# Kernel optimization log

Measured on AMD Instinct MI355X. Metric: run time of the kernel, lower is better.

## Reference

```python
import jax, jax.numpy as jnp
import numpy as np

L = 256
UP = 2
# ktype -> (rotations, ((pad_top,pad_bot),(pad_left,pad_right)), (b_row_off, b_col_off))
CONFIG = {
    'h': ([0, 2],        ((0, 0), (0, 1)), (0, 1)),
    'd': ([0, 1, 2, 3],  ((0, 1), (0, 1)), (1, 1)),
    'v': ([0, 2],        ((0, 1), (0, 0)), (1, 0)),
}


def setup_inputs() -> dict:
    key = jax.random.key(0)
    k0, k1, k2, k3 = jax.random.split(key, 4)
    img_lr = jax.random.randint(k0, (32, 1, 512, 512), 0, L, dtype=jnp.int32)
    h_weight = jax.random.normal(k1, (L * L, UP * UP), dtype=jnp.float32)
    d_weight = jax.random.normal(k2, (L * L, UP * UP), dtype=jnp.float32)
    v_weight = jax.random.normal(k3, (L * L, UP * UP), dtype=jnp.float32)
    return {"img_lr": img_lr, "h_weight": h_weight, "d_weight": d_weight, "v_weight": v_weight}


def reference(img_lr, h_weight, d_weight, v_weight):
    B, C, H0, W0 = img_lr.shape
    weights = {'h': h_weight, 'd': d_weight, 'v': v_weight}
    out = jnp.zeros((B, C, H0 * UP, W0 * UP), dtype=jnp.float32)
    for ktype in ('h', 'd', 'v'):
        rots, (ph, pw), (dr, dc) = CONFIG[ktype]
        w = weights[ktype].reshape(L * L, UP, UP)
        for r in rots:
            rot = jnp.rot90(img_lr, r, axes=(2, 3))
            H, W = rot.shape[2], rot.shape[3]
            padded = jnp.pad(rot, ((0, 0), (0, 0), ph, pw), mode='edge').astype(jnp.int32)
            img_a = padded[:, :, 0:H, 0:W]
            img_b = padded[:, :, dr:dr + H, dc:dc + W]
            # LUT gather: [B,C,H,W,UP,UP]
            tmp = w[img_a * L + img_b]
            # interleave subpixels: (B,C,H,uh,W,uw) -> (B,C,H*UP,W*UP)
            tmp = tmp.transpose(0, 1, 2, 4, 3, 5).reshape(B, C, H * UP, W * UP)
            out = out + jnp.rot90(tmp, (4 - r) % 4, axes=(2, 3))
    return out / 2.0
```

## Files before the change

kernel.cpp:

```cpp
#include <hip/hip_runtime.h>


typedef _Float16 h8 __attribute__((ext_vector_type(8)));
typedef _Float16 h4 __attribute__((ext_vector_type(4)));
typedef unsigned u32x2 __attribute__((ext_vector_type(2)));
typedef float    f32x2 __attribute__((ext_vector_type(2)));

#define WS_C(ws)     ((unsigned*)((char*)(ws) + 0x0))
#define WS_O(ws)     ((unsigned*)((char*)(ws) + 0x40000))
#define WS_T(ws)     ((unsigned*)((char*)(ws) + 0x80000))
#define WS_LUT16(ws) ((h4*)((char*)(ws) + 0x100000))
#define WS_SMAP(ws)  ((unsigned*)((char*)(ws) + 0x280000))
#define WS_RECS(ws)  ((u32x2*)((char*)(ws) + 0x2280000))
#define WS_AB(ws)    ((unsigned char*)((char*)(ws) + 0x6280000))
#define WS_NEED_BKT2 0x6A80000ull

__global__ __launch_bounds__(256) void p2_lut16(
    const float4* __restrict__ wh,
    const float4* __restrict__ wv,
    const float4* __restrict__ wd,
    h4* __restrict__ lut16)
{
    int idx = blockIdx.x * 256 + threadIdx.x;
    int l = idx >> 16, pq = idx & 65535;
    const float4* src = (l == 0) ? wh : (l == 1) ? wv : wd;
    float4 f = src[pq];
    h4 e;
    e[0] = (_Float16)f.x; e[1] = (_Float16)f.y;
    e[2] = (_Float16)f.z; e[3] = (_Float16)f.w;
    lut16[idx] = e;
}

__global__ __launch_bounds__(256) void p2_hist(
    const int* __restrict__ img, unsigned* __restrict__ C)
{
    __shared__ unsigned lh[32];
    int t = threadIdx.x;
    if (t < 32) lh[t] = 0u;
    __syncthreads();
    size_t base = (size_t)blockIdx.x * 4096;
    for (int k = 0; k < 16; ++k) {
        int a = img[base + (size_t)k * 256 + t];
        atomicAdd(&lh[a >> 3], 1u);
    }
    __syncthreads();
    if (t < 32) C[blockIdx.x * 32 + t] = lh[t];
}

__global__ __launch_bounds__(256) void p2_offsets(
    const unsigned* __restrict__ C, unsigned* __restrict__ O,
    unsigned* __restrict__ T)
{
    __shared__ unsigned tot[32], base[32];
    int imgb = blockIdx.x, t = threadIdx.x;
    if (t < 32) {
        unsigned run = 0;
        for (int blk = 0; blk < 64; ++blk) {
            int i = (imgb * 64 + blk) * 32 + t;
            unsigned c = C[i];
            O[i] = run;
            run += c;
        }
        tot[t] = run;
    }
    __syncthreads();
    if (t == 0) {
        unsigned run = 0;
        for (int g = 0; g < 32; ++g) {
            base[g] = (unsigned)(imgb * 262144) + run;
            run += tot[g];
        }
    }
    __syncthreads();
    if (t < 32) T[imgb * 32 + t] = tot[t];
    for (int k = 0; k < 8; ++k) {
        int i = k * 256 + t;
        O[imgb * 2048 + i] += base[i & 31];
    }
}

__global__ __launch_bounds__(256) void p2_scatter(
    const int* __restrict__ img, const unsigned* __restrict__ O,
    unsigned* __restrict__ SMAP, u32x2* __restrict__ RECS,
    unsigned char* __restrict__ AB)
{
    __shared__ unsigned lcur[32];
    int t = threadIdx.x;
    int blk = blockIdx.x;
    int imgb = blk >> 6;
    if (t < 32) lcur[t] = O[blk * 32 + t];
    __syncthreads();
    const int* I = img + ((size_t)imgb << 18);
    int pbase = (blk & 63) * 4096;
    for (int k = 0; k < 16; ++k) {
        int p = pbase + k * 256 + t;
        int x = p & 511, y = p >> 9;
        int xm = (x > 0) ? x - 1 : 0, xp = (x < 511) ? x + 1 : 511;
        int ym = (y > 0) ? y - 1 : 0, yp = (y < 511) ? y + 1 : 511;
        int rM = y << 9, rN = ym << 9, rS = yp << 9;
        unsigned a  = (unsigned)I[rM + x];
        unsigned E  = (unsigned)I[rM + xp], W_ = (unsigned)I[rM + xm];
        unsigned S  = (unsigned)I[rS + x ], N_ = (unsigned)I[rN + x ];
        unsigned SE = (unsigned)I[rS + xp], SW = (unsigned)I[rS + xm];
        unsigned NW = (unsigned)I[rN + xm], NE = (unsigned)I[rN + xp];
        unsigned slot = atomicAdd(&lcur[a >> 3], 1u);
        u32x2 r;
        r[0] = E  | (W_ << 8) | (S  << 16) | (N_ << 24);
        r[1] = SE | (SW << 8) | (NW << 16) | (NE << 24);
        RECS[slot] = r;
        AB[slot] = (unsigned char)(a & 7u);
        SMAP[(size_t)blk * 4096 + (size_t)k * 256 + t] = slot;
    }
}

__global__ __launch_bounds__(256) void p2_compute(
    const h4* __restrict__ LUT16, const unsigned* __restrict__ O,
    const unsigned* __restrict__ T, u32x2* __restrict__ RECS,
    const unsigned char* __restrict__ AB)
{
    __shared__ h4 sh[3][8][256];
    int t = threadIdx.x;
    int bid = blockIdx.x;
    int imgb = bid / 96;
    int r = bid - imgb * 96;
    int g = r / 3, c = r - (r / 3) * 3;
    unsigned start0 = O[(imgb * 64 + 0) * 32 + g];
    unsigned cnt    = T[imgb * 32 + g];
    unsigned start  = start0 + (unsigned)c * 4096u;
    unsigned end    = start0 + cnt;
    if (start >= end) return;

    for (int l = 0; l < 3; ++l)
        for (int j = 0; j < 8; ++j)
            sh[l][j][t] = LUT16[l * 65536 + ((g * 8 + j) << 8) + t];
    __syncthreads();

    h4* RESH = (h4*)RECS;
    for (int k = 0; k < 16; ++k) {
        unsigned slot = start + (unsigned)k * 256u + (unsigned)t;
        if (slot >= end) break;
        u32x2 rec = __builtin_nontemporal_load(&RECS[slot]);
        int j = AB[slot];
        unsigned n0 = rec[0], n1 = rec[1];
        h4 t4; float ax, ay, az, aw;
        t4 = sh[0][j][n0 & 255];         ax  = (float)t4[0]; ay  = (float)t4[1]; az  = (float)t4[2]; aw  = (float)t4[3];
        t4 = sh[0][j][(n0 >> 8) & 255];  ax += (float)t4[3]; ay += (float)t4[2]; az += (float)t4[1]; aw += (float)t4[0];
        t4 = sh[1][j][(n0 >> 16) & 255]; ax += (float)t4[0]; ay += (float)t4[1]; az += (float)t4[2]; aw += (float)t4[3];
        t4 = sh[1][j][n0 >> 24];         ax += (float)t4[3]; ay += (float)t4[2]; az += (float)t4[1]; aw += (float)t4[0];
        t4 = sh[2][j][n1 & 255];         ax += (float)t4[0]; ay += (float)t4[1]; az += (float)t4[2]; aw += (float)t4[3];
        t4 = sh[2][j][(n1 >> 8) & 255];  ax += (float)t4[2]; ay += (float)t4[0]; az += (float)t4[3]; aw += (float)t4[1];
        t4 = sh[2][j][(n1 >> 16) & 255]; ax += (float)t4[3]; ay += (float)t4[2]; az += (float)t4[1]; aw += (float)t4[0];
        t4 = sh[2][j][n1 >> 24];         ax += (float)t4[1]; ay += (float)t4[3]; az += (float)t4[0]; aw += (float)t4[2];
        h4 res;
        res[0] = (_Float16)(ax * 0.5f); res[1] = (_Float16)(ay * 0.5f);
        res[2] = (_Float16)(az * 0.5f); res[3] = (_Float16)(aw * 0.5f);
        RESH[slot] = res;
    }
}

__global__ __launch_bounds__(256) void p2_unsort(
    const unsigned* __restrict__ SMAP, const u32x2* __restrict__ RECS,
    float* __restrict__ out)
{
    int bid = blockIdx.x;
    int xcd = bid & 7;
    int rest = bid >> 3;
    int imgb = xcd * 4 + (rest >> 7);
    int within = rest & 127;
    int t = threadIdx.x;
    const h4* R = (const h4*)RECS;
    const unsigned* SM = SMAP + (size_t)imgb * 262144;
    for (int k = 0; k < 8; ++k) {
        int p = within * 2048 + k * 256 + t;
        unsigned slot = __builtin_nontemporal_load(&SM[p]);
        h4 res = R[slot];
        int x = p & 511, y = p >> 9;
        size_t obase = ((((size_t)imgb << 10) + (size_t)(y << 1)) << 10) + (size_t)(x << 1);
        f32x2 lo; lo[0] = (float)res[0]; lo[1] = (float)res[1];
        f32x2 hi; hi[0] = (float)res[2]; hi[1] = (float)res[3];
        __builtin_nontemporal_store(lo, (f32x2*)(out + obase));
        __builtin_nontemporal_store(hi, (f32x2*)(out + obase + 1024));
    }
}

__global__ __launch_bounds__(256) void hdvlut_prep(
    const float4* __restrict__ wh,
    const float4* __restrict__ wd,
    const float4* __restrict__ wv,
    h8* __restrict__ ws)
{
    int idx = blockIdx.x * 256 + threadIdx.x;
    int lut = idx >> 16;
    int pq  = idx & 65535;
    int p = pq >> 8, q = pq & 255;
    const float4* src = (lut == 0) ? wh : (lut == 1) ? wv : wd;
    float4 f = src[pq];
    float4 g = src[(q << 8) | p];
    h8 e;
    e[0] = (_Float16)f.x; e[1] = (_Float16)f.y;
    e[2] = (_Float16)f.z; e[3] = (_Float16)f.w;
    e[4] = (_Float16)g.x; e[5] = (_Float16)g.y;
    e[6] = (_Float16)g.z; e[7] = (_Float16)g.w;
    ws[idx] = e;
}

__global__ __launch_bounds__(256) void hdvlut_merged(
    const int* __restrict__ img,
    const h8* __restrict__ W2,
    float* __restrict__ out)
{
    __shared__ h4 bwdE[256], bwdS[256], bwdSE[256], bwdSW[256];

    int t  = threadIdx.x;
    int tx = t & 15, ty = t >> 4;
    int blk   = blockIdx.x;
    int tileX = blk & 31;
    int tileY = (blk >> 5) & 31;
    int b     = blk >> 10;
    int x = (tileX << 4) | tx;
    int y = (tileY << 4) | ty;

    const int* I = img + ((size_t)b << 18);

    int xm = (x > 0)   ? x - 1 : 0;
    int xp = (x < 511) ? x + 1 : 511;
    int ym = (y > 0)   ? y - 1 : 0;
    int yp = (y < 511) ? y + 1 : 511;
    int rM = y << 9, rN = ym << 9, rS = yp << 9;

    int a   = I[rM + x];
    int aE  = I[rM + xp], aW  = I[rM + xm];
    int aS  = I[rS + x ], aN  = I[rN + x ];
    int aSE = I[rS + xp], aSW = I[rS + xm];
    int aNW = I[rN + xm], aNE = I[rN + xp];
    int aL = a << 8;

    const h8* H2 = W2;
    const h8* V2 = W2 + 65536;
    const h8* D2 = W2 + 131072;

    h8 fE  = H2[aL + aE ];
    h8 fS  = V2[aL + aS ];
    h8 fSE = D2[aL + aSE];
    h8 fSW = D2[aL + aSW];

    bool bW  = (tx == 0);
    bool bN  = (ty == 0);
    bool bNW = bN || bW;
    bool bNE = bN || (tx == 15);
    h8 dW = {}, dN = {}, dNW = {}, dNE = {};
    if (bW)  dW  = H2[aL + aW ];
    if (bN)  dN  = V2[aL + aN ];
    if (bNW) dNW = D2[aL + aNW];
    if (bNE) dNE = D2[aL + aNE];

    bwdE [t] = __builtin_shufflevector(fE,  fE,  4, 5, 6, 7);
    bwdS [t] = __builtin_shufflevector(fS,  fS,  4, 5, 6, 7);
    bwdSE[t] = __builtin_shufflevector(fSE, fSE, 4, 5, 6, 7);
    bwdSW[t] = __builtin_shufflevector(fSW, fSW, 4, 5, 6, 7);
    __syncthreads();

    int txm = (tx > 0)  ? tx - 1 : 0;
    int txp = (tx < 15) ? tx + 1 : 15;
    int tym = (ty > 0)  ? ty - 1 : 0;
    h4 lW  = bwdE [(ty  << 4) | txm];
    h4 lN  = bwdS [(tym << 4) | tx ];
    h4 lNW = bwdSE[(tym << 4) | txm];
    h4 lNE = bwdSW[(tym << 4) | txp];

    h4 vW  = bW  ? __builtin_shufflevector(dW,  dW,  0, 1, 2, 3) : lW;
    h4 vN  = bN  ? __builtin_shufflevector(dN,  dN,  0, 1, 2, 3) : lN;
    h4 vNW = bNW ? __builtin_shufflevector(dNW, dNW, 0, 1, 2, 3) : lNW;
    h4 vNE = bNE ? __builtin_shufflevector(dNE, dNE, 0, 1, 2, 3) : lNE;

    float ax, ay, az, aw;
    ax  = (float)fE[0];  ay  = (float)fE[1];  az  = (float)fE[2];  aw  = (float)fE[3];
    ax += (float)fS[0];  ay += (float)fS[1];  az += (float)fS[2];  aw += (float)fS[3];
    ax += (float)fSE[0]; ay += (float)fSE[1]; az += (float)fSE[2]; aw += (float)fSE[3];
    ax += (float)fSW[2]; ay += (float)fSW[0]; az += (float)fSW[3]; aw += (float)fSW[1];
    ax += (float)vW[3];  ay += (float)vW[2];  az += (float)vW[1];  aw += (float)vW[0];
    ax += (float)vN[3];  ay += (float)vN[2];  az += (float)vN[1];  aw += (float)vN[0];
    ax += (float)vNW[3]; ay += (float)vNW[2]; az += (float)vNW[1]; aw += (float)vNW[0];
    ax += (float)vNE[1]; ay += (float)vNE[3]; az += (float)vNE[0]; aw += (float)vNE[2];

    size_t obase = ((((size_t)b << 10) + (y << 1)) << 10) + (x << 1);
    *(float2*)(out + obase)        = make_float2(ax * 0.5f, ay * 0.5f);
    *(float2*)(out + obase + 1024) = make_float2(az * 0.5f, aw * 0.5f);
}

__global__ __launch_bounds__(256) void hdvlut_plain(
    const int* __restrict__ img,
    const float4* __restrict__ wh,
    const float4* __restrict__ wd,
    const float4* __restrict__ wv,
    float* __restrict__ out)
{
    int idx = blockIdx.x * 256 + threadIdx.x;
    int x = idx & 511, y = (idx >> 9) & 511, b = idx >> 18;
    const int* I = img + ((size_t)b << 18);
    int row = y << 9;
    int xm = (x > 0) ? x - 1 : 0, xp = (x < 511) ? x + 1 : 511;
    int ym = (y > 0) ? y - 1 : 0, yp = (y < 511) ? y + 1 : 511;
    int rN = ym << 9, rS = yp << 9;
    int a = I[row|x], E = I[row|xp], W_ = I[row|xm], S = I[rS|x], N_ = I[rN|x];
    int SE = I[rS|xp], SW = I[rS|xm], NW = I[rN|xm], NE = I[rN|xp];
    int aL = a << 8;
    float4 t; float ax, ay, az, aw;
    t = wh[aL+E ]; ax  = t.x; ay  = t.y; az  = t.z; aw  = t.w;
    t = wh[aL+W_]; ax += t.w; ay += t.z; az += t.y; aw += t.x;
    t = wv[aL+S ]; ax += t.x; ay += t.y; az += t.z; aw += t.w;
    t = wv[aL+N_]; ax += t.w; ay += t.z; az += t.y; aw += t.x;
    t = wd[aL+SE]; ax += t.x; ay += t.y; az += t.z; aw += t.w;
    t = wd[aL+SW]; ax += t.z; ay += t.x; az += t.w; aw += t.y;
    t = wd[aL+NW]; ax += t.w; ay += t.z; az += t.y; aw += t.x;
    t = wd[aL+NE]; ax += t.y; ay += t.w; az += t.x; aw += t.z;
    size_t obase = ((((size_t)b << 10) + (y << 1)) << 10) + (x << 1);
    *(float2*)(out + obase)        = make_float2(ax*0.5f, ay*0.5f);
    *(float2*)(out + obase + 1024) = make_float2(az*0.5f, aw*0.5f);
}

extern "C" void kernel_launch(void* const* d_in, const int* in_sizes, int n_in,
                              void* d_out, int out_size, void* d_ws, size_t ws_size,
                              hipStream_t stream) {
    const int*    img = (const int*)d_in[0];
    const float4* wh  = (const float4*)d_in[1];
    const float4* wd  = (const float4*)d_in[2];
    const float4* wv  = (const float4*)d_in[3];
    float* out = (float*)d_out;

    int total = in_sizes[0];
    size_t need_merged = (size_t)3 * 65536 * 16;

    if (ws_size >= WS_NEED_BKT2 && (total >> 18) == 32) {
        hipLaunchKernelGGL(p2_lut16,   dim3(768),  dim3(256), 0, stream,
                           wh, wv, wd, WS_LUT16(d_ws));
        hipLaunchKernelGGL(p2_hist,    dim3(2048), dim3(256), 0, stream,
                           img, WS_C(d_ws));
        hipLaunchKernelGGL(p2_offsets, dim3(32),   dim3(256), 0, stream,
                           WS_C(d_ws), WS_O(d_ws), WS_T(d_ws));
        hipLaunchKernelGGL(p2_scatter, dim3(2048), dim3(256), 0, stream,
                           img, WS_O(d_ws), WS_SMAP(d_ws), WS_RECS(d_ws), WS_AB(d_ws));
        hipLaunchKernelGGL(p2_compute, dim3(3072), dim3(256), 0, stream,
                           WS_LUT16(d_ws), WS_O(d_ws), WS_T(d_ws), WS_RECS(d_ws), WS_AB(d_ws));
        hipLaunchKernelGGL(p2_unsort,  dim3(4096), dim3(256), 0, stream,
                           WS_SMAP(d_ws), WS_RECS(d_ws), out);
    } else if (ws_size >= need_merged) {
        h8* W2 = (h8*)d_ws;
        hipLaunchKernelGGL(hdvlut_prep, dim3(768), dim3(256), 0, stream,
                           wh, wd, wv, W2);
        hipLaunchKernelGGL(hdvlut_merged, dim3(total / 256), dim3(256), 0, stream,
                           img, W2, out);
    } else {
        hipLaunchKernelGGL(hdvlut_plain, dim3(total / 256), dim3(256), 0, stream,
                           img, wh, wd, wv, out);
    }
}
```

Measured before the change: 314.6 us.

## Fuse histogram, offsets and scatter into one tiled bucket-sort kernel

Replaces the three-kernel histogram, prefix-offset and scatter sequence with one sort kernel. That kernel stages a 66x66 halo tile of the image in LDS and reserves its bucket ranges through global atomic cursors, with a fixed capacity per bucket. Results go to a separate RES buffer rather than overwriting the record array. The unsort kernel now handles two pixels per thread and writes 16-byte stores. The aim is fewer launches, fewer redundant global neighbour reads and fewer passes over the image. In exchange it needs a much larger workspace, and it assumes no bucket exceeds 12288 entries.

Result: faster. 274.9 us (-12.6%).

```diff
diff --git a/kernel.cpp b/kernel.cpp
--- a/kernel.cpp
+++ b/kernel.cpp
@@ -4,16 +4,24 @@
 typedef _Float16 h8 __attribute__((ext_vector_type(8)));
 typedef _Float16 h4 __attribute__((ext_vector_type(4)));
 typedef unsigned u32x2 __attribute__((ext_vector_type(2)));
-typedef float    f32x2 __attribute__((ext_vector_type(2)));
-
-#define WS_C(ws)     ((unsigned*)((char*)(ws) + 0x0))
-#define WS_O(ws)     ((unsigned*)((char*)(ws) + 0x40000))
-#define WS_T(ws)     ((unsigned*)((char*)(ws) + 0x80000))
-#define WS_LUT16(ws) ((h4*)((char*)(ws) + 0x100000))
-#define WS_SMAP(ws)  ((unsigned*)((char*)(ws) + 0x280000))
-#define WS_RECS(ws)  ((u32x2*)((char*)(ws) + 0x2280000))
-#define WS_AB(ws)    ((unsigned char*)((char*)(ws) + 0x6280000))
-#define WS_NEED_BKT2 0x6A80000ull
+typedef float    f32x4 __attribute__((ext_vector_type(4)));
+
+#define P3_CURS(ws, i) (((unsigned*)(ws))[(size_t)(i) << 4])
+#define P3_LUT16(ws)   ((h4*)((char*)(ws) + 0x100000))
+#define P3_SMAP(ws)    ((unsigned*)((char*)(ws) + 0x280000))
+#define P3_RECS(ws)    ((u32x2*)((char*)(ws) + 0x2280000))
+#define P3_RES(ws)     ((h4*)((char*)(ws) + 0x8280000))
+#define P3_AB(ws)      ((unsigned char*)((char*)(ws) + 0xE280000))
+#define P3_NEED        0xEE80000ull
+#define P3_CAP         12288u
+
+__global__ __launch_bounds__(256) void p3_init(void* ws)
+{
+    for (int k = 0; k < 4; ++k) {
+        int i = k * 256 + threadIdx.x;
+        if (i < 1024) P3_CURS(ws, i) = (unsigned)i * P3_CAP;
+    }
+}
 
 __global__ __launch_bounds__(256) void p2_lut16(
     const float4* __restrict__ wh,
@@ -31,92 +39,61 @@
     lut16[idx] = e;
 }
 
-__global__ __launch_bounds__(256) void p2_hist(
-    const int* __restrict__ img, unsigned* __restrict__ C)
-{
-    __shared__ unsigned lh[32];
-    int t = threadIdx.x;
-    if (t < 32) lh[t] = 0u;
-    __syncthreads();
-    size_t base = (size_t)blockIdx.x * 4096;
-    for (int k = 0; k < 16; ++k) {
-        int a = img[base + (size_t)k * 256 + t];
-        atomicAdd(&lh[a >> 3], 1u);
-    }
-    __syncthreads();
-    if (t < 32) C[blockIdx.x * 32 + t] = lh[t];
-}
-
-__global__ __launch_bounds__(256) void p2_offsets(
-    const unsigned* __restrict__ C, unsigned* __restrict__ O,
-    unsigned* __restrict__ T)
-{
-    __shared__ unsigned tot[32], base[32];
-    int imgb = blockIdx.x, t = threadIdx.x;
-    if (t < 32) {
-        unsigned run = 0;
-        for (int blk = 0; blk < 64; ++blk) {
-            int i = (imgb * 64 + blk) * 32 + t;
-            unsigned c = C[i];
-            O[i] = run;
-            run += c;
-        }
-        tot[t] = run;
-    }
-    __syncthreads();
-    if (t == 0) {
-        unsigned run = 0;
-        for (int g = 0; g < 32; ++g) {
-            base[g] = (unsigned)(imgb * 262144) + run;
-            run += tot[g];
-        }
-    }
-    __syncthreads();
-    if (t < 32) T[imgb * 32 + t] = tot[t];
-    for (int k = 0; k < 8; ++k) {
-        int i = k * 256 + t;
-        O[imgb * 2048 + i] += base[i & 31];
-    }
-}
-
-__global__ __launch_bounds__(256) void p2_scatter(
-    const int* __restrict__ img, const unsigned* __restrict__ O,
-    unsigned* __restrict__ SMAP, u32x2* __restrict__ RECS,
-    unsigned char* __restrict__ AB)
-{
-    __shared__ unsigned lcur[32];
+__global__ __launch_bounds__(256) void p3_sort(
+    const int* __restrict__ img, void* ws)
+{
+    __shared__ int stage[66 * 66];
+    __shared__ unsigned lh[32], lbase[32], lcur[32];
     int t = threadIdx.x;
     int blk = blockIdx.x;
     int imgb = blk >> 6;
-    if (t < 32) lcur[t] = O[blk * 32 + t];
-    __syncthreads();
+    int tile = blk & 63;
+    int oy = (tile >> 3) << 6, ox = (tile & 7) << 6;
     const int* I = img + ((size_t)imgb << 18);
-    int pbase = (blk & 63) * 4096;
+
+    for (int l = t; l < 4356; l += 256) {
+        int ly = l / 66, lx = l - ly * 66;
+        int gy = oy + ly - 1; gy = (gy < 0) ? 0 : (gy > 511 ? 511 : gy);
+        int gx = ox + lx - 1; gx = (gx < 0) ? 0 : (gx > 511 ? 511 : gx);
+        stage[l] = I[(gy << 9) + gx];
+    }
+    if (t < 32) { lh[t] = 0u; lcur[t] = 0u; }
+    __syncthreads();
+
     for (int k = 0; k < 16; ++k) {
-        int p = pbase + k * 256 + t;
-        int x = p & 511, y = p >> 9;
-        int xm = (x > 0) ? x - 1 : 0, xp = (x < 511) ? x + 1 : 511;
-        int ym = (y > 0) ? y - 1 : 0, yp = (y < 511) ? y + 1 : 511;
-        int rM = y << 9, rN = ym << 9, rS = yp << 9;
-        unsigned a  = (unsigned)I[rM + x];
-        unsigned E  = (unsigned)I[rM + xp], W_ = (unsigned)I[rM + xm];
-        unsigned S  = (unsigned)I[rS + x ], N_ = (unsigned)I[rN + x ];
-        unsigned SE = (unsigned)I[rS + xp], SW = (unsigned)I[rS + xm];
-        unsigned NW = (unsigned)I[rN + xm], NE = (unsigned)I[rN + xp];
-        unsigned slot = atomicAdd(&lcur[a >> 3], 1u);
+        int l = k * 256 + t;
+        int ci = ((l >> 6) + 1) * 66 + (l & 63) + 1;
+        atomicAdd(&lh[((unsigned)stage[ci]) >> 3], 1u);
+    }
+    __syncthreads();
+    if (t < 32 && lh[t]) lbase[t] = atomicAdd(&P3_CURS(ws, imgb * 32 + t), lh[t]);
+    __syncthreads();
+
+    u32x2* RECS = P3_RECS(ws);
+    unsigned char* AB = P3_AB(ws);
+    unsigned* SMAP = P3_SMAP(ws) + (size_t)imgb * 262144;
+    for (int k = 0; k < 16; ++k) {
+        int l = k * 256 + t;
+        int ly = l >> 6, lx = l & 63;
+        int ci = (ly + 1) * 66 + lx + 1;
+        unsigned a  = (unsigned)stage[ci];
+        unsigned E  = (unsigned)stage[ci + 1],  W_ = (unsigned)stage[ci - 1];
+        unsigned S  = (unsigned)stage[ci + 66], N_ = (unsigned)stage[ci - 66];
+        unsigned SE = (unsigned)stage[ci + 67], SW = (unsigned)stage[ci + 65];
+        unsigned NW = (unsigned)stage[ci - 67], NE = (unsigned)stage[ci - 65];
+        unsigned g = a >> 3;
+        unsigned slot = lbase[g] + atomicAdd(&lcur[g], 1u);
         u32x2 r;
         r[0] = E  | (W_ << 8) | (S  << 16) | (N_ << 24);
         r[1] = SE | (SW << 8) | (NW << 16) | (NE << 24);
         RECS[slot] = r;
         AB[slot] = (unsigned char)(a & 7u);
-        SMAP[(size_t)blk * 4096 + (size_t)k * 256 + t] = slot;
-    }
-}
-
-__global__ __launch_bounds__(256) void p2_compute(
-    const h4* __restrict__ LUT16, const unsigned* __restrict__ O,
-    const unsigned* __restrict__ T, u32x2* __restrict__ RECS,
-    const unsigned char* __restrict__ AB)
+        SMAP[((oy + ly) << 9) + ox + lx] = slot;
+    }
+}
+
+__global__ __launch_bounds__(256) void p3_compute(
+    const h4* __restrict__ LUT16, void* ws)
 {
     __shared__ h4 sh[3][8][256];
     int t = threadIdx.x;
@@ -124,21 +101,22 @@
     int imgb = bid / 96;
     int r = bid - imgb * 96;
     int g = r / 3, c = r - (r / 3) * 3;
-    unsigned start0 = O[(imgb * 64 + 0) * 32 + g];
-    unsigned cnt    = T[imgb * 32 + g];
-    unsigned start  = start0 + (unsigned)c * 4096u;
-    unsigned end    = start0 + cnt;
-    if (start >= end) return;
+    unsigned base = (unsigned)(imgb * 32 + g) * P3_CAP;
+    unsigned endv = P3_CURS(ws, imgb * 32 + g);
+    unsigned start = base + (unsigned)c * 4096u;
+    if (start >= endv) return;
 
     for (int l = 0; l < 3; ++l)
         for (int j = 0; j < 8; ++j)
             sh[l][j][t] = LUT16[l * 65536 + ((g * 8 + j) << 8) + t];
     __syncthreads();
 
-    h4* RESH = (h4*)RECS;
+    u32x2* RECS = P3_RECS(ws);
+    h4* RES = P3_RES(ws);
+    const unsigned char* AB = P3_AB(ws);
     for (int k = 0; k < 16; ++k) {
         unsigned slot = start + (unsigned)k * 256u + (unsigned)t;
-        if (slot >= end) break;
+        if (slot >= endv) break;
         u32x2 rec = __builtin_nontemporal_load(&RECS[slot]);
         int j = AB[slot];
         unsigned n0 = rec[0], n1 = rec[1];
@@ -154,13 +132,12 @@
         h4 res;
         res[0] = (_Float16)(ax * 0.5f); res[1] = (_Float16)(ay * 0.5f);
         res[2] = (_Float16)(az * 0.5f); res[3] = (_Float16)(aw * 0.5f);
-        RESH[slot] = res;
-    }
-}
-
-__global__ __launch_bounds__(256) void p2_unsort(
-    const unsigned* __restrict__ SMAP, const u32x2* __restrict__ RECS,
-    float* __restrict__ out)
+        RES[slot] = res;
+    }
+}
+
+__global__ __launch_bounds__(256) void p3_unsort(
+    void* ws, float* __restrict__ out)
 {
     int bid = blockIdx.x;
     int xcd = bid & 7;
@@ -168,18 +145,23 @@
     int imgb = xcd * 4 + (rest >> 7);
     int within = rest & 127;
     int t = threadIdx.x;
-    const h4* R = (const h4*)RECS;
-    const unsigned* SM = SMAP + (size_t)imgb * 262144;
-    for (int k = 0; k < 8; ++k) {
-        int p = within * 2048 + k * 256 + t;
-        unsigned slot = __builtin_nontemporal_load(&SM[p]);
-        h4 res = R[slot];
+    const unsigned* SM = P3_SMAP(ws) + (size_t)imgb * 262144;
+    const h4* RES = P3_RES(ws);
+    for (int k = 0; k < 4; ++k) {
+        int pair = within * 1024 + k * 256 + t;
+        int p = pair << 1;
+        u32x2 ss = *(const u32x2*)(SM + p);
+        h4 r0 = RES[ss[0]];
+        h4 r1 = RES[ss[1]];
         int x = p & 511, y = p >> 9;
         size_t obase = ((((size_t)imgb << 10) + (size_t)(y << 1)) << 10) + (size_t)(x << 1);
-        f32x2 lo; lo[0] = (float)res[0]; lo[1] = (float)res[1];
-        f32x2 hi; hi[0] = (float)res[2]; hi[1] = (float)res[3];
-        __builtin_nontemporal_store(lo, (f32x2*)(out + obase));
-        __builtin_nontemporal_store(hi, (f32x2*)(out + obase + 1024));
+        f32x4 row0, row1;
+        row0[0] = (float)r0[0]; row0[1] = (float)r0[1];
+        row0[2] = (float)r1[0]; row0[3] = (float)r1[1];
+        row1[0] = (float)r0[2]; row1[1] = (float)r0[3];
+        row1[2] = (float)r1[2]; row1[3] = (float)r1[3];
+        __builtin_nontemporal_store(row0, (f32x4*)(out + obase));
+        __builtin_nontemporal_store(row1, (f32x4*)(out + obase + 1024));
     }
 }
 
@@ -331,19 +313,16 @@
     int total = in_sizes[0];
     size_t need_merged = (size_t)3 * 65536 * 16;
 
-    if (ws_size >= WS_NEED_BKT2 && (total >> 18) == 32) {
+    if (ws_size >= P3_NEED && (total >> 18) == 32) {
+        hipLaunchKernelGGL(p3_init,    dim3(1),    dim3(256), 0, stream, d_ws);
         hipLaunchKernelGGL(p2_lut16,   dim3(768),  dim3(256), 0, stream,
-                           wh, wv, wd, WS_LUT16(d_ws));
-        hipLaunchKernelGGL(p2_hist,    dim3(2048), dim3(256), 0, stream,
-                           img, WS_C(d_ws));
-        hipLaunchKernelGGL(p2_offsets, dim3(32),   dim3(256), 0, stream,
-                           WS_C(d_ws), WS_O(d_ws), WS_T(d_ws));
-        hipLaunchKernelGGL(p2_scatter, dim3(2048), dim3(256), 0, stream,
-                           img, WS_O(d_ws), WS_SMAP(d_ws), WS_RECS(d_ws), WS_AB(d_ws));
-        hipLaunchKernelGGL(p2_compute, dim3(3072), dim3(256), 0, stream,
-                           WS_LUT16(d_ws), WS_O(d_ws), WS_T(d_ws), WS_RECS(d_ws), WS_AB(d_ws));
-        hipLaunchKernelGGL(p2_unsort,  dim3(4096), dim3(256), 0, stream,
-                           WS_SMAP(d_ws), WS_RECS(d_ws), out);
+                           wh, wv, wd, P3_LUT16(d_ws));
+        hipLaunchKernelGGL(p3_sort,    dim3(2048), dim3(256), 0, stream,
+                           img, d_ws);
+        hipLaunchKernelGGL(p3_compute, dim3(3072), dim3(256), 0, stream,
+                           P3_LUT16(d_ws), d_ws);
+        hipLaunchKernelGGL(p3_unsort,  dim3(4096), dim3(256), 0, stream,
+                           d_ws, out);
     } else if (ws_size >= need_merged) {
         h8* W2 = (h8*)d_ws;
         hipLaunchKernelGGL(hdvlut_prep, dim3(768), dim3(256), 0, stream,
```
